# Optimization experiments

Measured on AMD Instinct MI355X. Metric: run time of the kernel, lower is better.

The kernel has to match this reference:

```python
import jax, jax.numpy as jnp
import numpy as np

N_NODES = 100000


def gcn_conv(x, edge_index, edge_weight, W, b):
    """PyG GCNConv: out = D^-1/2 (A + I) D^-1/2 X W + b (self-loop weight 1)."""
    n = x.shape[0]
    src, dst = edge_index[0], edge_index[1]
    loop = jnp.arange(n)
    src_sl = jnp.concatenate([src, loop])
    dst_sl = jnp.concatenate([dst, loop])
    ew_sl = jnp.concatenate([edge_weight, jnp.ones((n,), x.dtype)])
    deg = jax.ops.segment_sum(ew_sl, dst_sl, num_segments=n)  # [N]
    dinv = jnp.where(deg > 0, jax.lax.rsqrt(deg), 0.0)
    norm = dinv[src_sl] * ew_sl * dinv[dst_sl]  # [E+N]
    h = x @ W  # [N, out_dim] dense transform before propagation
    msg = h[src_sl] * norm[:, None]  # gather + scale, [E+N, out_dim]
    out = jax.ops.segment_sum(msg, dst_sl, num_segments=n)  # scatter-add
    return out + b


def setup_inputs() -> dict:
    key = jax.random.key(0)
    ks = jax.random.split(key, 9)
    in_dim, hidden, latent = 128, 64, 32
    n, e = N_NODES, 1600000
    x = jax.random.normal(ks[0], (n, in_dim), dtype=jnp.float32)
    edge_index = jax.random.randint(ks[1], (2, e), 0, n, dtype=jnp.int64)
    edge_weight = jax.random.uniform(ks[2], (e,), dtype=jnp.float32)
    def glorot(k, fan_in, fan_out):
        s = jnp.sqrt(6.0 / (fan_in + fan_out))
        return jax.random.uniform(k, (fan_in, fan_out), jnp.float32, -s, s)
    return {
        "x": x,
        "edge_index": edge_index,
        "edge_weight": edge_weight,
        "W1": glorot(ks[3], in_dim, hidden),
        "b1": jnp.zeros((hidden,), jnp.float32),
        "W_mu": glorot(ks[4], hidden, latent),
        "b_mu": jnp.zeros((latent,), jnp.float32),
        "W_lv": glorot(ks[5], hidden, latent),
        "b_lv": jnp.zeros((latent,), jnp.float32),
    }


def reference(x, edge_index, edge_weight, W1, b1, W_mu, b_mu, W_lv, b_lv):
    h = jax.nn.relu(gcn_conv(x, edge_index, edge_weight, W1, b1))
    mu = gcn_conv(h, edge_index, edge_weight, W_mu, b_mu)
    logvar = gcn_conv(h, edge_index, edge_weight, W_lv, b_lv)
    return (mu, logvar)
```

## Files before the change

### kernel.cpp

```cpp
#include <hip/hip_runtime.h>

static __device__ __forceinline__ float4 ld4(const float* p) { return *(const float4*)p; }
static __device__ __forceinline__ float b2f(unsigned short u) {
    return __uint_as_float((unsigned)u << 16);
}
static __device__ __forceinline__ float b2f_lo(unsigned u) { return __uint_as_float(u << 16); }
static __device__ __forceinline__ float b2f_hi(unsigned u) { return __uint_as_float(u & 0xFFFF0000u); }
static __device__ __forceinline__ unsigned short f2b(float f) {
    unsigned x = __float_as_uint(f);
    return (unsigned short)((x + 0x7FFFu + ((x >> 16) & 1u)) >> 16);
}
static __device__ __forceinline__ unsigned pk2(float lo, float hi) {
    return (unsigned)f2b(lo) | ((unsigned)f2b(hi) << 16);
}

#define NPB 256
#define CAPE 5120



__global__ __launch_bounds__(256) void k_fused1(const float* __restrict__ A,
                                                const float* __restrict__ W0,
                                                unsigned short* __restrict__ gout,
                                                const int* __restrict__ src,
                                                const int* __restrict__ dst,
                                                const float* __restrict__ ew,
                                                int* __restrict__ bin_cnt,
                                                unsigned long long* __restrict__ ebuf,
                                                int n, int E, int gb, int NB) {
    __shared__ float Ws[64 * 64];
    __shared__ float Xs[128 * 64];
    __shared__ int hist[512];
    __shared__ int hbase[512];
    int tid = threadIdx.x;

    if ((int)blockIdx.x < gb) {
        int row0 = blockIdx.x * 128;
        int c0 = (tid & 15) * 4;
        int rb = tid >> 4;
        int r0 = rb * 8;
        int swz = rb * 4;
        float4 acc[8] = {};
        #pragma unroll
        for (int p = 0; p < 2; p++) {
            for (int j = tid; j < 1024; j += 256)
                *(float4*)&Ws[j * 4] = ld4(W0 + p * 4096 + j * 4);
            for (int j = tid; j < 2048; j += 256) {
                int r = j >> 4, kc = (j & 15) * 4;
                int grow = row0 + r;
                float4 v = make_float4(0.f, 0.f, 0.f, 0.f);
                if (grow < n) v = ld4(A + (size_t)grow * 128 + p * 64 + kc);
                int sw = ((r >> 3) & 15) * 4;
                *(float4*)&Xs[r * 64 + (kc ^ sw)] = v;
            }
            __syncthreads();
            #pragma unroll 2
            for (int kk = 0; kk < 64; kk += 4) {
                float4 w0 = ld4(&Ws[(kk + 0) * 64 + c0]);
                float4 w1 = ld4(&Ws[(kk + 1) * 64 + c0]);
                float4 w2 = ld4(&Ws[(kk + 2) * 64 + c0]);
                float4 w3 = ld4(&Ws[(kk + 3) * 64 + c0]);
                #pragma unroll
                for (int i = 0; i < 8; i++) {
                    float4 a = ld4(&Xs[(r0 + i) * 64 + (kk ^ swz)]);
                    acc[i].x = fmaf(a.x, w0.x, fmaf(a.y, w1.x, fmaf(a.z, w2.x, fmaf(a.w, w3.x, acc[i].x))));
                    acc[i].y = fmaf(a.x, w0.y, fmaf(a.y, w1.y, fmaf(a.z, w2.y, fmaf(a.w, w3.y, acc[i].y))));
                    acc[i].z = fmaf(a.x, w0.z, fmaf(a.y, w1.z, fmaf(a.z, w2.z, fmaf(a.w, w3.z, acc[i].z))));
                    acc[i].w = fmaf(a.x, w0.w, fmaf(a.y, w1.w, fmaf(a.z, w2.w, fmaf(a.w, w3.w, acc[i].w))));
                }
            }
            __syncthreads();
        }
        #pragma unroll
        for (int i = 0; i < 8; i++) {
            int grow = row0 + r0 + i;
            if (grow < n) {
                ushort4 u = make_ushort4(f2b(acc[i].x), f2b(acc[i].y), f2b(acc[i].z), f2b(acc[i].w));
                *(ushort4*)&gout[(size_t)grow * 64 + c0] = u;
            }
        }
    } else {
        for (int j = tid; j < NB; j += 256) hist[j] = 0;
        __syncthreads();
        int e0 = ((int)blockIdx.x - gb) * 4096;
        unsigned long long pk[16]; int bb[16]; int loc[16];
        #pragma unroll
        for (int j = 0; j < 16; j++) {
            int e = e0 + j * 256 + tid;
            if (e < E) {
                int s = src[e];
                int d = dst[e];
                float w = ew[e];
                bb[j] = d >> 8;
                pk[j] = ((unsigned long long)__float_as_uint(w) << 32) |
                        (unsigned)((d & (NPB - 1)) << 17) | (unsigned)s;
                loc[j] = atomicAdd(&hist[bb[j]], 1);
            } else bb[j] = -1;
        }
        __syncthreads();
        for (int j = tid; j < NB; j += 256) hbase[j] = atomicAdd(&bin_cnt[j], hist[j]);
        __syncthreads();
        #pragma unroll
        for (int j = 0; j < 16; j++) {
            if (bb[j] >= 0)
                ebuf[(size_t)bb[j] * CAPE + hbase[bb[j]] + loc[j]] = pk[j];
        }
    }
}

__global__ __launch_bounds__(512) void k_csr_build(const unsigned long long* __restrict__ ebuf,
                                                   const int* __restrict__ bin_cnt,
                                                   int2* __restrict__ rowcnt,
                                                   float* __restrict__ dinv,
                                                   unsigned long long* __restrict__ csr,
                                                   unsigned short* __restrict__ h0,
                                                   int n) {
    __shared__ unsigned long long eL[CAPE];
    __shared__ unsigned cntL[NPB];
    __shared__ unsigned ewsL[NPB];
    __shared__ unsigned fillL[NPB];
    __shared__ int scanL[512];
    __shared__ int rowL[NPB];
    __shared__ float dinvL[NPB];
    __shared__ int binbase_s;
    int b = blockIdx.x;
    int tid = threadIdx.x;
    if (tid < NPB) { cntL[tid] = 0; ewsL[tid] = 0; fillL[tid] = 0; }
    scanL[tid] = (tid < b) ? bin_cnt[tid] : 0;
    __syncthreads();
    int m = bin_cnt[b];
    const unsigned long long* eb = ebuf + (size_t)b * CAPE;
    for (int i = tid; i < m; i += 512) {
        unsigned long long pk = eb[i];
        eL[i] = pk;
        int ld = (int)((pk >> 17) & (NPB - 1));
        float w = __uint_as_float((unsigned)(pk >> 32));
        atomicAdd(&cntL[ld], 1u);
        atomicAdd(&ewsL[ld], (unsigned)(w * 16777216.0f));
    }
    __syncthreads();
    #pragma unroll
    for (int off = 256; off > 0; off >>= 1) {
        if (tid < off) scanL[tid] += scanL[tid + off];
        __syncthreads();
    }
    if (tid == 0) binbase_s = scanL[0];
    __syncthreads();
    int v = (tid < NPB) ? (int)cntL[tid] : 0;
    scanL[tid] = v;
    __syncthreads();
    #pragma unroll
    for (int off = 1; off < 512; off <<= 1) {
        int t = (tid >= off) ? scanL[tid - off] : 0;
        __syncthreads();
        scanL[tid] += t;
        __syncthreads();
    }
    if (tid < NPB) {
        int rp = binbase_s + scanL[tid] - v;
        rowL[tid] = rp;
        float dv = rsqrtf(1.0f + (float)ewsL[tid] * (1.0f / 16777216.0f));
        dinvL[tid] = dv;
        int node = b * NPB + tid;
        if (node < n) {
            rowcnt[node] = make_int2(rp, v);
            dinv[node] = dv;
        }
    }
    __syncthreads();
    for (int i = tid; i < m; i += 512) {
        unsigned long long pk = eL[i];
        int s = (int)(pk & 0x1FFFF);
        int ld = (int)((pk >> 17) & (NPB - 1));
        int pos = rowL[ld] + (int)atomicAdd(&fillL[ld], 1u);
        csr[pos] = (unsigned long long)(unsigned)s | (pk & 0xFFFFFFFF00000000ull);
    }
    for (int idx = tid; idx < NPB * 8; idx += 512) {
        int ln = idx >> 3;
        int node = b * NPB + ln;
        if (node < n) {
            float sc = dinvL[ln];
            unsigned short* hp = h0 + (size_t)node * 64 + (idx & 7) * 8;
            uint4 u = *(uint4*)hp;
            u.x = pk2(b2f_lo(u.x) * sc, b2f_hi(u.x) * sc);
            u.y = pk2(b2f_lo(u.y) * sc, b2f_hi(u.y) * sc);
            u.z = pk2(b2f_lo(u.z) * sc, b2f_hi(u.z) * sc);
            u.w = pk2(b2f_lo(u.w) * sc, b2f_hi(u.w) * sc);
            *(uint4*)hp = u;
        }
    }
}

__global__ __launch_bounds__(256) void k_gemm2(const unsigned short* __restrict__ h,
                                               const float* __restrict__ Wmu,
                                               const float* __restrict__ Wlv,
                                               const float* __restrict__ dinv,
                                               unsigned short* __restrict__ out, int n) {
    __shared__ float Ws[64 * 64];
    __shared__ float Xs[128 * 64];
    int tid = threadIdx.x;
    int row0 = blockIdx.x * 128;
    for (int j = tid; j < 1024; j += 256) {
        int k = (j * 4) >> 6;
        int c = (j * 4) & 63;
        float4 v = (c < 32) ? ld4(Wmu + k * 32 + c) : ld4(Wlv + k * 32 + (c - 32));
        *(float4*)&Ws[j * 4] = v;
    }
    for (int j = tid; j < 1024; j += 256) {
        int r = j >> 3, ko = (j & 7) * 8;
        int grow = row0 + r;
        uint4 u = make_uint4(0u, 0u, 0u, 0u);
        if (grow < n) u = *(const uint4*)(h + (size_t)grow * 64 + ko);
        int sw = ((r >> 3) & 15) * 4;
        float4 v0 = make_float4(b2f_lo(u.x), b2f_hi(u.x), b2f_lo(u.y), b2f_hi(u.y));
        float4 v1 = make_float4(b2f_lo(u.z), b2f_hi(u.z), b2f_lo(u.w), b2f_hi(u.w));
        *(float4*)&Xs[r * 64 + (ko ^ sw)] = v0;
        *(float4*)&Xs[r * 64 + ((ko + 4) ^ sw)] = v1;
    }
    __syncthreads();

    int c0 = (tid & 15) * 4;
    int rb = tid >> 4;
    int r0 = rb * 8;
    int swz = rb * 4;
    float4 acc[8] = {};
    #pragma unroll 2
    for (int kk = 0; kk < 64; kk += 4) {
        float4 w0 = ld4(&Ws[(kk + 0) * 64 + c0]);
        float4 w1 = ld4(&Ws[(kk + 1) * 64 + c0]);
        float4 w2 = ld4(&Ws[(kk + 2) * 64 + c0]);
        float4 w3 = ld4(&Ws[(kk + 3) * 64 + c0]);
        #pragma unroll
        for (int i = 0; i < 8; i++) {
            float4 a = ld4(&Xs[(r0 + i) * 64 + (kk ^ swz)]);
            acc[i].x = fmaf(a.x, w0.x, fmaf(a.y, w1.x, fmaf(a.z, w2.x, fmaf(a.w, w3.x, acc[i].x))));
            acc[i].y = fmaf(a.x, w0.y, fmaf(a.y, w1.y, fmaf(a.z, w2.y, fmaf(a.w, w3.y, acc[i].y))));
            acc[i].z = fmaf(a.x, w0.z, fmaf(a.y, w1.z, fmaf(a.z, w2.z, fmaf(a.w, w3.z, acc[i].z))));
            acc[i].w = fmaf(a.x, w0.w, fmaf(a.y, w1.w, fmaf(a.z, w2.w, fmaf(a.w, w3.w, acc[i].w))));
        }
    }
    #pragma unroll
    for (int i = 0; i < 8; i++) {
        int grow = row0 + r0 + i;
        if (grow < n) {
            float sc = dinv[grow];
            ushort4 u = make_ushort4(f2b(acc[i].x * sc), f2b(acc[i].y * sc),
                                     f2b(acc[i].z * sc), f2b(acc[i].w * sc));
            *(ushort4*)&out[(size_t)grow * 64 + c0] = u;
        }
    }
}

static __device__ __forceinline__ void acc8(float* a, uint4 r, float wt) {
    a[0] = fmaf(b2f_lo(r.x), wt, a[0]); a[1] = fmaf(b2f_hi(r.x), wt, a[1]);
    a[2] = fmaf(b2f_lo(r.y), wt, a[2]); a[3] = fmaf(b2f_hi(r.y), wt, a[3]);
    a[4] = fmaf(b2f_lo(r.z), wt, a[4]); a[5] = fmaf(b2f_hi(r.z), wt, a[5]);
    a[6] = fmaf(b2f_lo(r.w), wt, a[6]); a[7] = fmaf(b2f_hi(r.w), wt, a[7]);
}

template<bool RELU, bool SPLIT_OUT>
__global__ __launch_bounds__(256) void k_prop(const unsigned short* __restrict__ g,
                                              const int2* __restrict__ csr,
                                              const int2* __restrict__ rowcnt,
                                              const float* __restrict__ dinv,
                                              const float* __restrict__ bias0,
                                              const float* __restrict__ bias1,
                                              void* __restrict__ outv, int n) {
    int node = blockIdx.x * 4 + (threadIdx.x >> 6);
    if (node >= n) return;
    int lane = threadIdx.x & 63;
    int q = lane >> 3;
    int t = lane & 7;
    uint4 sr = *(const uint4*)(g + (size_t)node * 64 + t * 8);
    int2 rc = rowcnt[node];
    const int2* ep = csr + rc.x;
    int m = rc.y;
    float a[8] = {};
    for (int e = 0; e < m; e += 32) {
        int e1 = e + q, e2 = e1 + 8, e3 = e1 + 16, e4 = e1 + 24;
        int i1 = min(e1, m - 1), i2 = min(e2, m - 1);
        int i3 = min(e3, m - 1), i4 = min(e4, m - 1);
        int2 p1 = ep[i1];
        int2 p2 = ep[i2];
        int2 p3 = ep[i3];
        int2 p4 = ep[i4];
        uint4 r1 = *(const uint4*)(g + (size_t)p1.x * 64 + t * 8);
        uint4 r2 = *(const uint4*)(g + (size_t)p2.x * 64 + t * 8);
        uint4 r3 = *(const uint4*)(g + (size_t)p3.x * 64 + t * 8);
        uint4 r4 = *(const uint4*)(g + (size_t)p4.x * 64 + t * 8);
        float w1 = (e1 < m) ? __int_as_float(p1.y) : 0.f;
        float w2 = (e2 < m) ? __int_as_float(p2.y) : 0.f;
        float w3 = (e3 < m) ? __int_as_float(p3.y) : 0.f;
        float w4 = (e4 < m) ? __int_as_float(p4.y) : 0.f;
        acc8(a, r1, w1);
        acc8(a, r2, w2);
        acc8(a, r3, w3);
        acc8(a, r4, w4);
    }
    #pragma unroll
    for (int i = 0; i < 8; i++) {
        a[i] += __shfl_xor(a[i], 8);
        a[i] += __shfl_xor(a[i], 16);
        a[i] += __shfl_xor(a[i], 32);
    }
    if (q != 0) return;
    a[0] += b2f_lo(sr.x); a[1] += b2f_hi(sr.x);
    a[2] += b2f_lo(sr.y); a[3] += b2f_hi(sr.y);
    a[4] += b2f_lo(sr.z); a[5] += b2f_hi(sr.z);
    a[6] += b2f_lo(sr.w); a[7] += b2f_hi(sr.w);
    float di = dinv[node];
    #pragma unroll
    for (int i = 0; i < 8; i++) a[i] *= di;
    if (!SPLIT_OUT) {
        float4 b0 = ld4(bias0 + t * 8);
        float4 b1 = ld4(bias0 + t * 8 + 4);
        a[0] += b0.x; a[1] += b0.y; a[2] += b0.z; a[3] += b0.w;
        a[4] += b1.x; a[5] += b1.y; a[6] += b1.z; a[7] += b1.w;
        if (RELU) {
            #pragma unroll
            for (int i = 0; i < 8; i++) a[i] = fmaxf(a[i], 0.f);
        }
        uint4 u = make_uint4(pk2(a[0], a[1]), pk2(a[2], a[3]),
                             pk2(a[4], a[5]), pk2(a[6], a[7]));
        *(uint4*)((unsigned short*)outv + (size_t)node * 64 + t * 8) = u;
    } else {
        float* out = (float*)outv;
        const float* bp = (t < 4) ? (bias0 + t * 8) : (bias1 + (t - 4) * 8);
        size_t base = (t < 4) ? ((size_t)node * 32 + t * 8)
                              : ((size_t)n * 32 + (size_t)node * 32 + (t - 4) * 8);
        float4 b0 = ld4(bp);
        float4 b1 = ld4(bp + 4);
        float4 v0 = make_float4(a[0] + b0.x, a[1] + b0.y, a[2] + b0.z, a[3] + b0.w);
        float4 v1 = make_float4(a[4] + b1.x, a[5] + b1.y, a[6] + b1.z, a[7] + b1.w);
        *(float4*)&out[base] = v0;
        *(float4*)&out[base + 4] = v1;
    }
}

extern "C" void kernel_launch(void* const* d_in, const int* in_sizes, int n_in,
                              void* d_out, int out_size, void* d_ws, size_t ws_size,
                              hipStream_t stream) {
    const float* x   = (const float*)d_in[0];
    const int*   ei  = (const int*)d_in[1];
    const float* ew  = (const float*)d_in[2];
    const float* W1  = (const float*)d_in[3];
    const float* b1  = (const float*)d_in[4];
    const float* Wmu = (const float*)d_in[5];
    const float* bmu = (const float*)d_in[6];
    const float* Wlv = (const float*)d_in[7];
    const float* blv = (const float*)d_in[8];
    float* outp = (float*)d_out;

    const int n = in_sizes[0] / 128;
    const int E = in_sizes[2];
    const int* src = ei;
    const int* dst = ei + E;
    const int NB = (n + NPB - 1) / NPB;

    size_t o = 0;
    auto alloc = [&](size_t bytes) { void* p = (char*)d_ws + o; o += (bytes + 511) & ~(size_t)511; return p; };
    int*   bin_cnt  = (int*)alloc((size_t)NB * 4);
    int2*  rowcnt   = (int2*)alloc((size_t)n * 8);
    float* dinv     = (float*)alloc((size_t)n * 4);
    unsigned long long* csr  = (unsigned long long*)alloc((size_t)E * 8);
    unsigned long long* ebuf = (unsigned long long*)alloc((size_t)NB * CAPE * 8);
    unsigned short* g0 = (unsigned short*)alloc((size_t)n * 64 * 2);
    unsigned short* h  = (unsigned short*)alloc((size_t)n * 64 * 2);
    unsigned short* g2 = g0;

    const int gb = (n + 127) / 128;
    const int bb = (E + 4095) / 4096;

    hipMemsetAsync(bin_cnt, 0, (size_t)NB * 4, stream);
    k_fused1<<<gb + bb, 256, 0, stream>>>(x, W1, g0, src, dst, ew,
                                          bin_cnt, ebuf, n, E, gb, NB);
    k_csr_build<<<NB, 512, 0, stream>>>(ebuf, bin_cnt, rowcnt, dinv, csr, g0, n);
    k_prop<true, false><<<(n + 3) / 4, 256, 0, stream>>>(g0, (const int2*)csr, rowcnt, dinv,
                                                         b1, nullptr, h, n);
    k_gemm2<<<gb, 256, 0, stream>>>(h, Wmu, Wlv, dinv, g2, n);
    k_prop<false, true><<<(n + 3) / 4, 256, 0, stream>>>(g2, (const int2*)csr, rowcnt, dinv,
                                                         bmu, blv, outp, n);
}
```

Baseline: 277.7 us.

## Use split-bf16 MFMA for both dense GEMMs instead of fp32 FMA

```diff
diff --git a/kernel.cpp b/kernel.cpp
--- a/kernel.cpp
+++ b/kernel.cpp
@@ -13,6 +13,9 @@
 static __device__ __forceinline__ unsigned pk2(float lo, float hi) {
     return (unsigned)f2b(lo) | ((unsigned)f2b(hi) << 16);
 }
+
+typedef __attribute__((ext_vector_type(8))) short bf16x8;
+typedef __attribute__((ext_vector_type(4))) float f32x4;
 
 #define NPB 256
 #define CAPE 5120
@@ -28,55 +31,70 @@
                                                 int* __restrict__ bin_cnt,
                                                 unsigned long long* __restrict__ ebuf,
                                                 int n, int E, int gb, int NB) {
-    __shared__ float Ws[64 * 64];
-    __shared__ float Xs[128 * 64];
+    __shared__ unsigned short xh[64 * 136];
+    __shared__ unsigned short xl[64 * 136];
+    __shared__ unsigned short Wth[64 * 136];
+    __shared__ unsigned short Wtl[64 * 136];
     __shared__ int hist[512];
     __shared__ int hbase[512];
     int tid = threadIdx.x;
 
     if ((int)blockIdx.x < gb) {
-        int row0 = blockIdx.x * 128;
-        int c0 = (tid & 15) * 4;
-        int rb = tid >> 4;
-        int r0 = rb * 8;
-        int swz = rb * 4;
-        float4 acc[8] = {};
-        #pragma unroll
-        for (int p = 0; p < 2; p++) {
-            for (int j = tid; j < 1024; j += 256)
-                *(float4*)&Ws[j * 4] = ld4(W0 + p * 4096 + j * 4);
-            for (int j = tid; j < 2048; j += 256) {
-                int r = j >> 4, kc = (j & 15) * 4;
-                int grow = row0 + r;
-                float4 v = make_float4(0.f, 0.f, 0.f, 0.f);
-                if (grow < n) v = ld4(A + (size_t)grow * 128 + p * 64 + kc);
-                int sw = ((r >> 3) & 15) * 4;
-                *(float4*)&Xs[r * 64 + (kc ^ sw)] = v;
+        int row0 = blockIdx.x * 64;
+        for (int j = tid; j < 2048; j += 256) {
+            int c = j >> 5, kq = (j & 31) * 4;
+            ushort4 uh, ul;
+            #pragma unroll
+            for (int i = 0; i < 4; i++) {
+                float wv = W0[(size_t)(kq + i) * 64 + c];
+                unsigned short hi = f2b(wv);
+                unsigned short lo = f2b(wv - b2f(hi));
+                ((unsigned short*)&uh)[i] = hi;
+                ((unsigned short*)&ul)[i] = lo;
             }
-            __syncthreads();
-            #pragma unroll 2
-            for (int kk = 0; kk < 64; kk += 4) {
-                float4 w0 = ld4(&Ws[(kk + 0) * 64 + c0]);
-                float4 w1 = ld4(&Ws[(kk + 1) * 64 + c0]);
-                float4 w2 = ld4(&Ws[(kk + 2) * 64 + c0]);
-                float4 w3 = ld4(&Ws[(kk + 3) * 64 + c0]);
+            *(ushort4*)&Wth[c * 136 + kq] = uh;
+            *(ushort4*)&Wtl[c * 136 + kq] = ul;
+        }
+        for (int j = tid; j < 2048; j += 256) {
+            int r = j >> 5, kc = (j & 31) * 4;
+            int grow = row0 + r;
+            float4 v = make_float4(0.f, 0.f, 0.f, 0.f);
+            if (grow < n) v = ld4(A + (size_t)grow * 128 + kc);
+            ushort4 uh, ul;
+            uh.x = f2b(v.x); ul.x = f2b(v.x - b2f(uh.x));
+            uh.y = f2b(v.y); ul.y = f2b(v.y - b2f(uh.y));
+            uh.z = f2b(v.z); ul.z = f2b(v.z - b2f(uh.z));
+            uh.w = f2b(v.w); ul.w = f2b(v.w - b2f(uh.w));
+            *(ushort4*)&xh[r * 136 + kc] = uh;
+            *(ushort4*)&xl[r * 136 + kc] = ul;
+        }
+        __syncthreads();
+        int w = tid >> 6, lane = tid & 63;
+        int rA = lane & 15;
+        int g8 = (lane >> 4) * 8;
+        f32x4 acc[4] = {{0.f, 0.f, 0.f, 0.f}, {0.f, 0.f, 0.f, 0.f},
+                        {0.f, 0.f, 0.f, 0.f}, {0.f, 0.f, 0.f, 0.f}};
+        #pragma unroll
+        for (int kb = 0; kb < 4; kb++) {
+            bf16x8 ah = *(const bf16x8*)&xh[(w * 16 + rA) * 136 + kb * 32 + g8];
+            bf16x8 al = *(const bf16x8*)&xl[(w * 16 + rA) * 136 + kb * 32 + g8];
+            #pragma unroll
+            for (int ct = 0; ct < 4; ct++) {
+                bf16x8 bh = *(const bf16x8*)&Wth[(ct * 16 + rA) * 136 + kb * 32 + g8];
+                bf16x8 bl = *(const bf16x8*)&Wtl[(ct * 16 + rA) * 136 + kb * 32 + g8];
+                acc[ct] = __builtin_amdgcn_mfma_f32_16x16x32_bf16(ah, bh, acc[ct], 0, 0, 0);
+                acc[ct] = __builtin_amdgcn_mfma_f32_16x16x32_bf16(al, bh, acc[ct], 0, 0, 0);
+                acc[ct] = __builtin_amdgcn_mfma_f32_16x16x32_bf16(ah, bl, acc[ct], 0, 0, 0);
+            }
+        }
+        int rbase = row0 + w * 16 + (lane >> 4) * 4;
+        #pragma unroll
+        for (int reg = 0; reg < 4; reg++) {
+            int grow = rbase + reg;
+            if (grow < n) {
                 #pragma unroll
-                for (int i = 0; i < 8; i++) {
-                    float4 a = ld4(&Xs[(r0 + i) * 64 + (kk ^ swz)]);
-                    acc[i].x = fmaf(a.x, w0.x, fmaf(a.y, w1.x, fmaf(a.z, w2.x, fmaf(a.w, w3.x, acc[i].x))));
-                    acc[i].y = fmaf(a.x, w0.y, fmaf(a.y, w1.y, fmaf(a.z, w2.y, fmaf(a.w, w3.y, acc[i].y))));
-                    acc[i].z = fmaf(a.x, w0.z, fmaf(a.y, w1.z, fmaf(a.z, w2.z, fmaf(a.w, w3.z, acc[i].z))));
-                    acc[i].w = fmaf(a.x, w0.w, fmaf(a.y, w1.w, fmaf(a.z, w2.w, fmaf(a.w, w3.w, acc[i].w))));
-                }
-            }
-            __syncthreads();
-        }
-        #pragma unroll
-        for (int i = 0; i < 8; i++) {
-            int grow = row0 + r0 + i;
-            if (grow < n) {
-                ushort4 u = make_ushort4(f2b(acc[i].x), f2b(acc[i].y), f2b(acc[i].z), f2b(acc[i].w));
-                *(ushort4*)&gout[(size_t)grow * 64 + c0] = u;
+                for (int ct = 0; ct < 4; ct++)
+                    gout[(size_t)grow * 64 + ct * 16 + rA] = f2b(acc[ct][reg]);
             }
         }
     } else {
@@ -196,57 +214,60 @@
                                                const float* __restrict__ Wlv,
                                                const float* __restrict__ dinv,
                                                unsigned short* __restrict__ out, int n) {
-    __shared__ float Ws[64 * 64];
-    __shared__ float Xs[128 * 64];
+    __shared__ unsigned short hA[64 * 72];
+    __shared__ unsigned short Wth[64 * 72];
+    __shared__ unsigned short Wtl[64 * 72];
     int tid = threadIdx.x;
-    int row0 = blockIdx.x * 128;
+    int row0 = blockIdx.x * 64;
     for (int j = tid; j < 1024; j += 256) {
-        int k = (j * 4) >> 6;
-        int c = (j * 4) & 63;
-        float4 v = (c < 32) ? ld4(Wmu + k * 32 + c) : ld4(Wlv + k * 32 + (c - 32));
-        *(float4*)&Ws[j * 4] = v;
-    }
-    for (int j = tid; j < 1024; j += 256) {
-        int r = j >> 3, ko = (j & 7) * 8;
+        int c = j >> 4, kq = (j & 15) * 4;
+        const float* Wsrc = (c < 32) ? Wmu : Wlv;
+        int cc = c & 31;
+        ushort4 uh, ul;
+        #pragma unroll
+        for (int i = 0; i < 4; i++) {
+            float wv = Wsrc[(size_t)(kq + i) * 32 + cc];
+            unsigned short hi = f2b(wv);
+            unsigned short lo = f2b(wv - b2f(hi));
+            ((unsigned short*)&uh)[i] = hi;
+            ((unsigned short*)&ul)[i] = lo;
+        }
+        *(ushort4*)&Wth[c * 72 + kq] = uh;
+        *(ushort4*)&Wtl[c * 72 + kq] = ul;
+    }
+    for (int j = tid; j < 512; j += 256) {
+        int r = j >> 3, q = (j & 7) * 8;
         int grow = row0 + r;
         uint4 u = make_uint4(0u, 0u, 0u, 0u);
-        if (grow < n) u = *(const uint4*)(h + (size_t)grow * 64 + ko);
-        int sw = ((r >> 3) & 15) * 4;
-        float4 v0 = make_float4(b2f_lo(u.x), b2f_hi(u.x), b2f_lo(u.y), b2f_hi(u.y));
-        float4 v1 = make_float4(b2f_lo(u.z), b2f_hi(u.z), b2f_lo(u.w), b2f_hi(u.w));
-        *(float4*)&Xs[r * 64 + (ko ^ sw)] = v0;
-        *(float4*)&Xs[r * 64 + ((ko + 4) ^ sw)] = v1;
-    }
-    __syncthreads();
-
-    int c0 = (tid & 15) * 4;
-    int rb = tid >> 4;
-    int r0 = rb * 8;
-    int swz = rb * 4;
-    float4 acc[8] = {};
-    #pragma unroll 2
-    for (int kk = 0; kk < 64; kk += 4) {
-        float4 w0 = ld4(&Ws[(kk + 0) * 64 + c0]);
-        float4 w1 = ld4(&Ws[(kk + 1) * 64 + c0]);
-        float4 w2 = ld4(&Ws[(kk + 2) * 64 + c0]);
-        float4 w3 = ld4(&Ws[(kk + 3) * 64 + c0]);
-        #pragma unroll
-        for (int i = 0; i < 8; i++) {
-            float4 a = ld4(&Xs[(r0 + i) * 64 + (kk ^ swz)]);
-            acc[i].x = fmaf(a.x, w0.x, fmaf(a.y, w1.x, fmaf(a.z, w2.x, fmaf(a.w, w3.x, acc[i].x))));
-            acc[i].y = fmaf(a.x, w0.y, fmaf(a.y, w1.y, fmaf(a.z, w2.y, fmaf(a.w, w3.y, acc[i].y))));
-            acc[i].z = fmaf(a.x, w0.z, fmaf(a.y, w1.z, fmaf(a.z, w2.z, fmaf(a.w, w3.z, acc[i].z))));
-            acc[i].w = fmaf(a.x, w0.w, fmaf(a.y, w1.w, fmaf(a.z, w2.w, fmaf(a.w, w3.w, acc[i].w))));
-        }
-    }
-    #pragma unroll
-    for (int i = 0; i < 8; i++) {
-        int grow = row0 + r0 + i;
+        if (grow < n) u = *(const uint4*)(h + (size_t)grow * 64 + q);
+        *(uint4*)&hA[r * 72 + q] = u;
+    }
+    __syncthreads();
+    int w = tid >> 6, lane = tid & 63;
+    int rA = lane & 15;
+    int g8 = (lane >> 4) * 8;
+    f32x4 acc[4] = {{0.f, 0.f, 0.f, 0.f}, {0.f, 0.f, 0.f, 0.f},
+                    {0.f, 0.f, 0.f, 0.f}, {0.f, 0.f, 0.f, 0.f}};
+    #pragma unroll
+    for (int kb = 0; kb < 2; kb++) {
+        bf16x8 a = *(const bf16x8*)&hA[(w * 16 + rA) * 72 + kb * 32 + g8];
+        #pragma unroll
+        for (int ct = 0; ct < 4; ct++) {
+            bf16x8 bh = *(const bf16x8*)&Wth[(ct * 16 + rA) * 72 + kb * 32 + g8];
+            bf16x8 bl = *(const bf16x8*)&Wtl[(ct * 16 + rA) * 72 + kb * 32 + g8];
+            acc[ct] = __builtin_amdgcn_mfma_f32_16x16x32_bf16(a, bh, acc[ct], 0, 0, 0);
+            acc[ct] = __builtin_amdgcn_mfma_f32_16x16x32_bf16(a, bl, acc[ct], 0, 0, 0);
+        }
+    }
+    int rbase = row0 + w * 16 + (lane >> 4) * 4;
+    #pragma unroll
+    for (int reg = 0; reg < 4; reg++) {
+        int grow = rbase + reg;
         if (grow < n) {
             float sc = dinv[grow];
-            ushort4 u = make_ushort4(f2b(acc[i].x * sc), f2b(acc[i].y * sc),
-                                     f2b(acc[i].z * sc), f2b(acc[i].w * sc));
-            *(ushort4*)&out[(size_t)grow * 64 + c0] = u;
+            #pragma unroll
+            for (int ct = 0; ct < 4; ct++)
+                out[(size_t)grow * 64 + ct * 16 + rA] = f2b(acc[ct][reg] * sc);
         }
     }
 }
@@ -368,7 +389,7 @@
     unsigned short* h  = (unsigned short*)alloc((size_t)n * 64 * 2);
     unsigned short* g2 = g0;
 
-    const int gb = (n + 127) / 128;
+    const int gb = (n + 63) / 64;
     const int bb = (E + 4095) / 4096;
 
     hipMemsetAsync(bin_cnt, 0, (size_t)NB * 4, stream);
```

New measurement: 288.8 us. +4.0%, slower.
